# Performance work log

Hardware: AMD Instinct MI355X
Metric: run time of the kernel (lower is better)

## Reference

```python
import jax, jax.numpy as jnp
import numpy as np
import math

S, B, D = 2048, 8, 256
HEADS = 8
DPROJ = 128
DFF = 1024
DH = DPROJ // HEADS  # 16


def _layernorm(x, g, b, eps=1e-5):
    mu = jnp.mean(x, axis=-1, keepdims=True)
    var = jnp.mean((x - mu) ** 2, axis=-1, keepdims=True)
    return (x - mu) * jax.lax.rsqrt(var + eps) * g + b


def setup_inputs() -> dict:
    key = jax.random.key(0)
    ks = jax.random.split(key, 16)
    s = 0.02
    return {
        "src": jax.random.normal(ks[0], (S, B, D), dtype=jnp.float32),
        "Wq": jax.random.normal(ks[1], (D, DPROJ), dtype=jnp.float32) * s,
        "bq": jnp.zeros((DPROJ,), dtype=jnp.float32),
        "Wk": jax.random.normal(ks[2], (D, DPROJ), dtype=jnp.float32) * s,
        "bk": jnp.zeros((DPROJ,), dtype=jnp.float32),
        "Wv": jax.random.normal(ks[3], (D, DPROJ), dtype=jnp.float32) * s,
        "bv": jnp.zeros((DPROJ,), dtype=jnp.float32),
        "Wo": jax.random.normal(ks[4], (DPROJ, D), dtype=jnp.float32) * s,
        "ln1_g": jnp.ones((D,), dtype=jnp.float32),
        "ln1_b": jnp.zeros((D,), dtype=jnp.float32),
        "W1": jax.random.normal(ks[5], (D, DFF), dtype=jnp.float32) * s,
        "b1": jnp.zeros((DFF,), dtype=jnp.float32),
        "W2": jax.random.normal(ks[6], (DFF, D), dtype=jnp.float32) * s,
        "b2": jnp.zeros((D,), dtype=jnp.float32),
        "ln2_g": jnp.ones((D,), dtype=jnp.float32),
        "ln2_b": jnp.zeros((D,), dtype=jnp.float32),
    }


def reference(src, Wq, bq, Wk, bk, Wv, bv, Wo, ln1_g, ln1_b, W1, b1, W2, b2, ln2_g, ln2_b):
    # src: (S, B, D)
    q = src @ Wq + bq  # (S, B, DPROJ)
    k = src @ Wk + bk
    v = src @ Wv + bv

    # _reshape_to_batches: (S, B, h*dh) -> (S, B*h, dh), then sdpa moves batch first
    def split_heads(x):
        return jnp.transpose(x.reshape(S, B * HEADS, DH), (1, 0, 2))  # (B*h, S, dh)

    qh, kh, vh = split_heads(q), split_heads(k), split_heads(v)
    scores = jnp.einsum('bid,bjd->bij', qh, kh) / math.sqrt(DH)  # (B*h, S, S)
    attn = jax.nn.softmax(scores, axis=-1)
    ctx = jnp.einsum('bij,bjd->bid', attn, vh)  # (B*h, S, dh)

    # _reshape_from_batches: (B*h, S, dh) -> (S, B, DPROJ)
    ctx = jnp.transpose(ctx, (1, 0, 2)).reshape(S, B, DPROJ)
    y = ctx @ Wo  # (S, B, D), no bias

    x = _layernorm(src + y, ln1_g, ln1_b)
    ffn = jax.nn.relu(x @ W1 + b1) @ W2 + b2
    return _layernorm(x + ffn, ln2_g, ln2_b)
```

## Files before the change

### kernel.cpp

```cpp
#include <hip/hip_runtime.h>
#include <math.h>

#define SLEN 2048
#define BATCH 8
#define DMODEL 256
#define HEADS 8
#define DPROJ 128
#define DFF 1024
#define DH 16
#define MROWS (SLEN*BATCH)

typedef unsigned short u16;
typedef unsigned int u32;
typedef __attribute__((ext_vector_type(8))) short short8;
typedef __attribute__((ext_vector_type(4))) float f32x4;
typedef __attribute__((ext_vector_type(16))) float f32x16;
typedef __attribute__((ext_vector_type(4))) unsigned short u16x4;

__device__ __forceinline__ u16 f2bf(float x) {
    union { float f; u32 u; } v; v.f = x;
    u32 r = v.u + 0x7FFFu + ((v.u >> 16) & 1u);
    return (u16)(r >> 16);
}
__device__ __forceinline__ float bf2f(u16 h) {
    union { u32 u; float f; } v; v.u = ((u32)h) << 16;
    return v.f;
}
__device__ __forceinline__ float fexp2(float x) { return __builtin_amdgcn_exp2f(x); }
__device__ __forceinline__ u32 pack_bf(float lo, float hi) {
    union { float f; u32 u; } a, b; a.f = lo; b.f = hi;
    return __builtin_amdgcn_perm(b.u, a.u, 0x07060302u);
}
__device__ __forceinline__ void gld16(const u16* g, u16* l) {
    __builtin_amdgcn_global_load_lds(
        (const __attribute__((address_space(1))) void*)g,
        (__attribute__((address_space(3))) void*)l, 16, 0, 0);
}

__global__ void prep_kernel(const float* __restrict__ src, u16* __restrict__ srcb,
                            const float* __restrict__ Wq, const float* __restrict__ Wk,
                            const float* __restrict__ Wv, const float* __restrict__ Wo,
                            const float* __restrict__ W1, const float* __restrict__ W2,
                            u16* __restrict__ WqT, u16* __restrict__ WkT,
                            u16* __restrict__ WvT, u16* __restrict__ WoT,
                            u16* __restrict__ W1T, u16* __restrict__ W2T) {
    if (blockIdx.x < 4096) {
        int idx = (blockIdx.x * 256 + threadIdx.x) * 4;
        float4 v = *(const float4*)(src + idx);
        u16x4 o;
        o.x = f2bf(v.x); o.y = f2bf(v.y); o.z = f2bf(v.z); o.w = f2bf(v.w);
        *(u16x4*)(srcb + idx) = o;
        return;
    }
    int i = (blockIdx.x - 4096) * 256 + threadIdx.x;
    if (i < 32768) {
        int n = i >> 8, k = i & 255;
        WqT[i] = f2bf(Wq[k * 128 + n]);
    } else if (i < 65536) {
        int j = i - 32768; int n = j >> 8, k = j & 255;
        WkT[j] = f2bf(Wk[k * 128 + n]);
    } else if (i < 98304) {
        int j = i - 65536; int n = j >> 8, k = j & 255;
        WvT[j] = f2bf(Wv[k * 128 + n]);
    } else if (i < 131072) {
        int j = i - 98304; int n = j >> 7, k = j & 127;
        WoT[j] = f2bf(Wo[k * 256 + n]);
    } else if (i < 393216) {
        int j = i - 131072; int n = j >> 8, k = j & 255;
        W1T[j] = f2bf(W1[k * 1024 + n]);
    } else if (i < 655360) {
        int j = i - 393216; int n = j >> 10, k = j & 1023;
        W2T[j] = f2bf(W2[k * 256 + n]);
    }
}

template<int BN, bool RELU, bool HAS_BIAS, bool OUT_BF16>
__global__ void mfma_gemm(const u16* __restrict__ A, const u16* __restrict__ BT,
                          const float* __restrict__ bias, void* __restrict__ Cout,
                          int M, int N, int K) {
    constexpr int NJ = BN / 32;
    __shared__ __align__(16) u16 As[128 * 32];
    __shared__ __align__(16) u16 Bs[BN * 32];
    const int tid = threadIdx.x;
    const int row0 = blockIdx.x * 128;
    const int col0 = blockIdx.y * BN;
    const int w = tid >> 6, l = tid & 63;
    const int wr = (w & 1) * 64, wc = (w >> 1) * (BN / 2);
    const int lcol = l & 15, lrow = (l >> 4) * 4, g = l >> 4;
    const int sl = l >> 2;
    const int swc = ((l & 3) ^ (sl & 3)) * 8;
    const int fsw = (g ^ (lcol & 3)) * 8;

    const u16* Ag0 = A + (size_t)(row0 + 16 * w + sl) * K + swc;
    const u16* Ag1 = Ag0 + (size_t)64 * K;
    const u16* Bg0 = BT + (size_t)(col0 + 16 * w + sl) * K + swc;
    const u16* Bg1 = Bg0 + (size_t)64 * K;
    u16* lA0 = As + (16 * w) * 32;
    u16* lA1 = As + (16 * w + 64) * 32;
    u16* lB0 = Bs + (16 * w) * 32;
    u16* lB1 = Bs + (16 * w + 64) * 32;

    f32x4 acc[4][NJ] = {};
    for (int k0 = 0; k0 < K; k0 += 32) {
        gld16(Ag0 + k0, lA0);
        gld16(Ag1 + k0, lA1);
        gld16(Bg0 + k0, lB0);
        if (BN == 128) gld16(Bg1 + k0, lB1);
        __syncthreads();
        short8 af[4], bf[NJ];
        #pragma unroll
        for (int i = 0; i < 4; ++i)
            af[i] = *(const short8*)(As + (wr + i * 16 + lcol) * 32 + fsw);
        #pragma unroll
        for (int j = 0; j < NJ; ++j)
            bf[j] = *(const short8*)(Bs + (wc + j * 16 + lcol) * 32 + fsw);
        #pragma unroll
        for (int i = 0; i < 4; ++i)
            #pragma unroll
            for (int j = 0; j < NJ; ++j)
                acc[i][j] = __builtin_amdgcn_mfma_f32_16x16x32_bf16(
                    af[i], bf[j], acc[i][j], 0, 0, 0);
        __syncthreads();
    }
    float bv[NJ];
    #pragma unroll
    for (int j = 0; j < NJ; ++j)
        bv[j] = HAS_BIAS ? bias[col0 + wc + j * 16 + lcol] : 0.f;
    #pragma unroll
    for (int i = 0; i < 4; ++i) {
        #pragma unroll
        for (int r = 0; r < 4; ++r) {
            size_t grow = row0 + wr + i * 16 + lrow + r;
            #pragma unroll
            for (int j = 0; j < NJ; ++j) {
                int gcol = col0 + wc + j * 16 + lcol;
                float c = acc[i][j][r] + bv[j];
                if (RELU) c = fmaxf(c, 0.f);
                if (OUT_BF16) ((u16*)Cout)[grow * N + gcol] = f2bf(c);
                else          ((float*)Cout)[grow * N + gcol] = c;
            }
        }
    }
}

__global__ void qkv_mfma(const u16* __restrict__ A,
                         const u16* __restrict__ WqT, const u16* __restrict__ WkT,
                         const u16* __restrict__ WvT,
                         const float* __restrict__ bq, const float* __restrict__ bk,
                         const float* __restrict__ bv,
                         u16* __restrict__ qhp, u16* __restrict__ khp,
                         u16* __restrict__ vhb) {
    const int which = blockIdx.z;
    const u16* BT   = which == 0 ? WqT : (which == 1 ? WkT : WvT);
    const float* bs = which == 0 ? bq : (which == 1 ? bk : bv);
    u16* outp       = which == 0 ? qhp : (which == 1 ? khp : vhb);
    const float scale = which == 0 ? 0.25f * 1.44269504f : 1.0f;
    __shared__ __align__(16) u16 As[128 * 32];
    __shared__ __align__(16) u16 Bs[128 * 32];
    const int tid = threadIdx.x;
    const int row0 = blockIdx.x * 128;
    const int w = tid >> 6, l = tid & 63;
    const int wr = (w & 1) * 64, wc = (w >> 1) * 64;
    const int lcol = l & 15, lrow = (l >> 4) * 4, g = l >> 4;
    const int sl = l >> 2;
    const int swc = ((l & 3) ^ (sl & 3)) * 8;
    const int fsw = (g ^ (lcol & 3)) * 8;

    const u16* Ag0 = A + (size_t)(row0 + 16 * w + sl) * DMODEL + swc;
    const u16* Ag1 = Ag0 + (size_t)64 * DMODEL;
    const u16* Bg0 = BT + (size_t)(16 * w + sl) * DMODEL + swc;
    const u16* Bg1 = Bg0 + (size_t)64 * DMODEL;
    u16* lA0 = As + (16 * w) * 32;
    u16* lA1 = As + (16 * w + 64) * 32;
    u16* lB0 = Bs + (16 * w) * 32;
    u16* lB1 = Bs + (16 * w + 64) * 32;

    f32x4 acc[4][4] = {};
    for (int k0 = 0; k0 < DMODEL; k0 += 32) {
        gld16(Ag0 + k0, lA0);
        gld16(Ag1 + k0, lA1);
        gld16(Bg0 + k0, lB0);
        gld16(Bg1 + k0, lB1);
        __syncthreads();
        short8 af[4], bf[4];
        #pragma unroll
        for (int i = 0; i < 4; ++i)
            af[i] = *(const short8*)(As + (wr + i * 16 + lcol) * 32 + fsw);
        #pragma unroll
        for (int j = 0; j < 4; ++j)
            bf[j] = *(const short8*)(Bs + (wc + j * 16 + lcol) * 32 + fsw);
        #pragma unroll
        for (int i = 0; i < 4; ++i)
            #pragma unroll
            for (int j = 0; j < 4; ++j)
                acc[i][j] = __builtin_amdgcn_mfma_f32_16x16x32_bf16(
                    af[i], bf[j], acc[i][j], 0, 0, 0);
        __syncthreads();
    }
    #pragma unroll
    for (int i = 0; i < 4; ++i) {
        #pragma unroll
        for (int r = 0; r < 4; ++r) {
            int grow = row0 + wr + i * 16 + lrow + r;
            int b = grow & 7, s = grow >> 3;
            #pragma unroll
            for (int j = 0; j < 4; ++j) {
                int gcol = wc + j * 16 + lcol;
                int h = gcol >> 4, d = gcol & 15;
                float c = acc[i][j][r] + bs[gcol];
                outp[((size_t)(b * 8 + h) * SLEN + s) * 16 + d] = f2bf(c * scale);
            }
        }
    }
}

__global__ void transpose_v(const u16* __restrict__ vhb, u16* __restrict__ va) {
    __shared__ u16 T[128 * 24];
    const int bh = blockIdx.y;
    const int c0 = blockIdx.x * 128;
    const int t = threadIdx.x;
    {
        int key = t >> 1, half = t & 1;
        *(uint4*)(T + key * 24 + half * 8) =
            *(const uint4*)(vhb + ((size_t)bh * SLEN + c0 + key) * 16 + half * 8);
    }
    __syncthreads();
    int d = t >> 4, k8 = (t & 15) * 8;
    u16x4 o0, o1;
    o0.x = T[(k8 + 0) * 24 + d]; o0.y = T[(k8 + 1) * 24 + d];
    o0.z = T[(k8 + 2) * 24 + d]; o0.w = T[(k8 + 3) * 24 + d];
    o1.x = T[(k8 + 4) * 24 + d]; o1.y = T[(k8 + 5) * 24 + d];
    o1.z = T[(k8 + 6) * 24 + d]; o1.w = T[(k8 + 7) * 24 + d];
    u16* dst = va + ((size_t)bh * 32 + d) * SLEN + c0 + k8;
    *(u16x4*)dst = o0;
    *(u16x4*)(dst + 4) = o1;
    if (t < 16) {
        u16x4 ones = { (u16)0x3F80, (u16)0x3F80, (u16)0x3F80, (u16)0x3F80 };
        u16* od = va + ((size_t)bh * 32 + 16) * SLEN + c0 + t * 8;
        *(u16x4*)od = ones;
        *(u16x4*)(od + 4) = ones;
    }
}

__global__ __launch_bounds__(256, 4)
void attn_mfma(const u16* __restrict__ qg, const u16* __restrict__ kg,
               const u16* __restrict__ va, u16* __restrict__ ctx) {
    __shared__ __align__(16) u16 Ps[4 * 2 * 32 * 72];
    const int bh = blockIdx.y;
    const int q0 = blockIdx.x * 128;
    const int tid = threadIdx.x;
    const int w = tid >> 6, l = tid & 63;
    const int n = l & 31, h5 = l >> 5;
    u16* Pbase = Ps + w * (2 * 32 * 72);

    const short8 qf = *(const short8*)(
        qg + ((size_t)bh * SLEN + q0 + w * 32 + n) * 16 + h5 * 8);
    const u16* kb = kg + (size_t)bh * SLEN * 16;
    const u16* vb = va + ((size_t)bh * 32 + n) * SLEN + h5 * 8;

    f32x16 oacc = {};

    short8 kf0 = *(const short8*)(kb + (size_t)n * 16 + h5 * 8);
    short8 kf1 = *(const short8*)(kb + (size_t)(32 + n) * 16 + h5 * 8);

    for (int kt = 0; kt < 32; ++kt) {
        const int k0 = kt * 64;
        u16* Pw = Pbase + (kt & 1) * (32 * 72);
        short8 vf[4];
        #pragma unroll
        for (int st = 0; st < 4; ++st)
            vf[st] = *(const short8*)(vb + k0 + st * 16);
        f32x16 z = {};
        f32x16 s0 = __builtin_amdgcn_mfma_f32_32x32x16_bf16(kf0, qf, z, 0, 0, 0);
        f32x16 s1 = __builtin_amdgcn_mfma_f32_32x32x16_bf16(kf1, qf, z, 0, 0, 0);
        const int kn = (kt < 31) ? (k0 + 64) : 0;
        kf0 = *(const short8*)(kb + (size_t)(kn + n) * 16 + h5 * 8);
        kf1 = *(const short8*)(kb + (size_t)(kn + 32 + n) * 16 + h5 * 8);
        #pragma unroll
        for (int r4 = 0; r4 < 4; ++r4) {
            uint2 d0, d1;
            d0.x = pack_bf(fexp2(s0[r4 * 4 + 0]), fexp2(s0[r4 * 4 + 1]));
            d0.y = pack_bf(fexp2(s0[r4 * 4 + 2]), fexp2(s0[r4 * 4 + 3]));
            d1.x = pack_bf(fexp2(s1[r4 * 4 + 0]), fexp2(s1[r4 * 4 + 1]));
            d1.y = pack_bf(fexp2(s1[r4 * 4 + 2]), fexp2(s1[r4 * 4 + 3]));
            int kbase = 8 * r4 + 4 * h5;
            *(uint2*)(Pw + n * 72 + kbase) = d0;
            *(uint2*)(Pw + n * 72 + 32 + kbase) = d1;
        }
        #pragma unroll
        for (int st = 0; st < 4; ++st) {
            short8 ap = *(const short8*)(Pw + n * 72 + st * 16 + h5 * 8);
            oacc = __builtin_amdgcn_mfma_f32_32x32x16_bf16(ap, vf[st], oacc, 0, 0, 0);
        }
    }
    float* Ob = (float*)Pbase;
    #pragma unroll
    for (int r = 0; r < 16; ++r) {
        int q = (r & 3) + 8 * (r >> 2) + 4 * h5;
        if (n <= 16) Ob[q * 36 + n] = oacc[r];
    }
    __syncthreads();
    const int q = l >> 1, half = l & 1;
    f32x4 o0 = *(const f32x4*)(Ob + q * 36 + half * 8);
    f32x4 o1 = *(const f32x4*)(Ob + q * 36 + half * 8 + 4);
    float rcpL = 1.0f / Ob[q * 36 + 16];
    u16x4 pa, pb;
    pa.x = f2bf(o0[0] * rcpL); pa.y = f2bf(o0[1] * rcpL);
    pa.z = f2bf(o0[2] * rcpL); pa.w = f2bf(o0[3] * rcpL);
    pb.x = f2bf(o1[0] * rcpL); pb.y = f2bf(o1[1] * rcpL);
    pb.z = f2bf(o1[2] * rcpL); pb.w = f2bf(o1[3] * rcpL);
    const int b = bh >> 3, h = bh & 7;
    const int qrow = q0 + w * 32 + q;
    u16* dst = ctx + ((size_t)qrow * BATCH + b) * DPROJ + h * DH + half * 8;
    *(u16x4*)dst = pa;
    *(u16x4*)(dst + 4) = pb;
}

__global__ void ln1_kernel(const float* __restrict__ src, const u16* __restrict__ y,
                           const float* __restrict__ g, const float* __restrict__ bb,
                           u16* __restrict__ xb) {
    const int w = threadIdx.x >> 6, l = threadIdx.x & 63;
    const int row = blockIdx.x * 4 + w;
    const int c = l * 4;
    size_t base = (size_t)row * DMODEL;
    float4 s4 = *(const float4*)(src + base + c);
    u16x4 y4 = *(const u16x4*)(y + base + c);
    float v[4] = { s4.x + bf2f(y4.x), s4.y + bf2f(y4.y),
                   s4.z + bf2f(y4.z), s4.w + bf2f(y4.w) };
    float sum = v[0] + v[1] + v[2] + v[3];
    float ss  = v[0]*v[0] + v[1]*v[1] + v[2]*v[2] + v[3]*v[3];
    #pragma unroll
    for (int off = 1; off < 64; off <<= 1) {
        sum += __shfl_xor(sum, off);
        ss  += __shfl_xor(ss, off);
    }
    float mu = sum * (1.0f / 256.0f);
    float var = ss * (1.0f / 256.0f) - mu * mu;
    float rs = rsqrtf(var + 1e-5f);
    float4 g4 = *(const float4*)(g + c);
    float4 b4 = *(const float4*)(bb + c);
    u16x4 o;
    o.x = f2bf((v[0] - mu) * rs * g4.x + b4.x);
    o.y = f2bf((v[1] - mu) * rs * g4.y + b4.y);
    o.z = f2bf((v[2] - mu) * rs * g4.z + b4.z);
    o.w = f2bf((v[3] - mu) * rs * g4.w + b4.w);
    *(u16x4*)(xb + base + c) = o;
}

__global__ void ln2_kernel(const u16* __restrict__ x, const u16* __restrict__ f,
                           const float* __restrict__ g, const float* __restrict__ bb,
                           float* __restrict__ out) {
    const int w = threadIdx.x >> 6, l = threadIdx.x & 63;
    const int row = blockIdx.x * 4 + w;
    const int c = l * 4;
    size_t base = (size_t)row * DMODEL;
    u16x4 x4 = *(const u16x4*)(x + base + c);
    u16x4 f4 = *(const u16x4*)(f + base + c);
    float v[4] = { bf2f(x4.x) + bf2f(f4.x), bf2f(x4.y) + bf2f(f4.y),
                   bf2f(x4.z) + bf2f(f4.z), bf2f(x4.w) + bf2f(f4.w) };
    float sum = v[0] + v[1] + v[2] + v[3];
    float ss  = v[0]*v[0] + v[1]*v[1] + v[2]*v[2] + v[3]*v[3];
    #pragma unroll
    for (int off = 1; off < 64; off <<= 1) {
        sum += __shfl_xor(sum, off);
        ss  += __shfl_xor(ss, off);
    }
    float mu = sum * (1.0f / 256.0f);
    float var = ss * (1.0f / 256.0f) - mu * mu;
    float rs = rsqrtf(var + 1e-5f);
    float4 g4 = *(const float4*)(g + c);
    float4 b4 = *(const float4*)(bb + c);
    float4 o;
    o.x = (v[0] - mu) * rs * g4.x + b4.x;
    o.y = (v[1] - mu) * rs * g4.y + b4.y;
    o.z = (v[2] - mu) * rs * g4.z + b4.z;
    o.w = (v[3] - mu) * rs * g4.w + b4.w;
    *(float4*)(out + base + c) = o;
}

extern "C" void kernel_launch(void* const* d_in, const int* in_sizes, int n_in,
                              void* d_out, int out_size, void* d_ws, size_t ws_size,
                              hipStream_t stream) {
    const float* src = (const float*)d_in[0];
    const float* Wq  = (const float*)d_in[1];
    const float* bq  = (const float*)d_in[2];
    const float* Wk  = (const float*)d_in[3];
    const float* bk  = (const float*)d_in[4];
    const float* Wv  = (const float*)d_in[5];
    const float* bv  = (const float*)d_in[6];
    const float* Wo  = (const float*)d_in[7];
    const float* g1  = (const float*)d_in[8];
    const float* be1 = (const float*)d_in[9];
    const float* W1  = (const float*)d_in[10];
    const float* b1  = (const float*)d_in[11];
    const float* W2  = (const float*)d_in[12];
    const float* b2  = (const float*)d_in[13];
    const float* g2  = (const float*)d_in[14];
    const float* be2 = (const float*)d_in[15];
    char* ws = (char*)d_ws;
    float* out = (float*)d_out;

    u16* qhp  = (u16*)(ws + 0);
    u16* khp  = (u16*)(ws + 4194304);
    u16* vhb  = (u16*)(ws + 8388608);
    u16* vaug = (u16*)(ws + 12582912);
    u16* ctxb = (u16*)(ws + 20971520);
    u16* yb   = (u16*)(ws + 25165824);
    u16* hb   = (u16*)(ws + 0);
    u16* xb   = (u16*)(ws + 33554432);
    u16* fb   = (u16*)(ws + 41943040);
    u16* srcb = (u16*)(ws + 50331648);
    u16* WqT  = (u16*)(ws + 58720256);
    u16* WkT  = (u16*)(ws + 58785792);
    u16* WvT  = (u16*)(ws + 58851328);
    u16* WoT  = (u16*)(ws + 58916864);
    u16* W1T  = (u16*)(ws + 58982400);
    u16* W2T  = (u16*)(ws + 59506688);

    prep_kernel<<<6656, 256, 0, stream>>>(src, srcb, Wq, Wk, Wv, Wo, W1, W2,
                                          WqT, WkT, WvT, WoT, W1T, W2T);
    qkv_mfma<<<dim3(128, 1, 3), 256, 0, stream>>>(srcb, WqT, WkT, WvT,
                                                  bq, bk, bv, qhp, khp, vhb);
    transpose_v<<<dim3(16, 64), 256, 0, stream>>>(vhb, vaug);
    attn_mfma<<<dim3(16, 64), 256, 0, stream>>>(qhp, khp, vaug, ctxb);
    mfma_gemm<64, false, false, true><<<dim3(128, 4), 256, 0, stream>>>(
        ctxb, WoT, nullptr, yb, MROWS, DMODEL, DPROJ);
    ln1_kernel<<<MROWS / 4, 256, 0, stream>>>(src, yb, g1, be1, xb);
    mfma_gemm<128, true, true, true><<<dim3(128, 8), 256, 0, stream>>>(
        xb, W1T, b1, hb, MROWS, DFF, DMODEL);
    mfma_gemm<64, false, true, true><<<dim3(128, 4), 256, 0, stream>>>(
        hb, W2T, b2, fb, MROWS, DMODEL, DFF);
    ln2_kernel<<<MROWS / 4, 256, 0, stream>>>(xb, fb, g2, be2, out);
}
```

Baseline: 240.4 us.

## Split attention over key halves and combine fp32 partials in separate kernel

```diff
diff --git a/kernel.cpp b/kernel.cpp
--- a/kernel.cpp
+++ b/kernel.cpp
@@ -9,6 +9,7 @@
 #define DFF 1024
 #define DH 16
 #define MROWS (SLEN*BATCH)
+#define NROWS (SLEN*BATCH*8)
 
 typedef unsigned short u16;
 typedef unsigned int u32;
@@ -242,30 +243,30 @@
     }
 }
 
-__global__ __launch_bounds__(256, 4)
+__global__ __launch_bounds__(128, 8)
 void attn_mfma(const u16* __restrict__ qg, const u16* __restrict__ kg,
-               const u16* __restrict__ va, u16* __restrict__ ctx) {
-    __shared__ __align__(16) u16 Ps[4 * 2 * 32 * 72];
+               const u16* __restrict__ va, float* __restrict__ part) {
+    __shared__ __align__(16) u16 Ps[2 * 32 * 68];
     const int bh = blockIdx.y;
-    const int q0 = blockIdx.x * 128;
+    const int sl = blockIdx.z;
     const int tid = threadIdx.x;
     const int w = tid >> 6, l = tid & 63;
     const int n = l & 31, h5 = l >> 5;
-    u16* Pbase = Ps + w * (2 * 32 * 72);
-
+    u16* Pw = Ps + w * (32 * 68);
+
+    const int qbase = blockIdx.x * 64 + w * 32;
     const short8 qf = *(const short8*)(
-        qg + ((size_t)bh * SLEN + q0 + w * 32 + n) * 16 + h5 * 8);
+        qg + ((size_t)bh * SLEN + qbase + n) * 16 + h5 * 8);
     const u16* kb = kg + (size_t)bh * SLEN * 16;
     const u16* vb = va + ((size_t)bh * 32 + n) * SLEN + h5 * 8;
+    const int k00 = sl * (SLEN / 2);
 
     f32x16 oacc = {};
-
-    short8 kf0 = *(const short8*)(kb + (size_t)n * 16 + h5 * 8);
-    short8 kf1 = *(const short8*)(kb + (size_t)(32 + n) * 16 + h5 * 8);
-
-    for (int kt = 0; kt < 32; ++kt) {
-        const int k0 = kt * 64;
-        u16* Pw = Pbase + (kt & 1) * (32 * 72);
+    short8 kf0 = *(const short8*)(kb + (size_t)(k00 + n) * 16 + h5 * 8);
+    short8 kf1 = *(const short8*)(kb + (size_t)(k00 + 32 + n) * 16 + h5 * 8);
+
+    for (int kt = 0; kt < 16; ++kt) {
+        const int k0 = k00 + kt * 64;
         short8 vf[4];
         #pragma unroll
         for (int st = 0; st < 4; ++st)
@@ -273,47 +274,61 @@
         f32x16 z = {};
         f32x16 s0 = __builtin_amdgcn_mfma_f32_32x32x16_bf16(kf0, qf, z, 0, 0, 0);
         f32x16 s1 = __builtin_amdgcn_mfma_f32_32x32x16_bf16(kf1, qf, z, 0, 0, 0);
-        const int kn = (kt < 31) ? (k0 + 64) : 0;
+        const int kn = k00 + ((kt + 1) & 15) * 64;
         kf0 = *(const short8*)(kb + (size_t)(kn + n) * 16 + h5 * 8);
         kf1 = *(const short8*)(kb + (size_t)(kn + 32 + n) * 16 + h5 * 8);
         #pragma unroll
         for (int r4 = 0; r4 < 4; ++r4) {
-            uint2 d0, d1;
-            d0.x = pack_bf(fexp2(s0[r4 * 4 + 0]), fexp2(s0[r4 * 4 + 1]));
-            d0.y = pack_bf(fexp2(s0[r4 * 4 + 2]), fexp2(s0[r4 * 4 + 3]));
-            d1.x = pack_bf(fexp2(s1[r4 * 4 + 0]), fexp2(s1[r4 * 4 + 1]));
-            d1.y = pack_bf(fexp2(s1[r4 * 4 + 2]), fexp2(s1[r4 * 4 + 3]));
-            int kbase = 8 * r4 + 4 * h5;
-            *(uint2*)(Pw + n * 72 + kbase) = d0;
-            *(uint2*)(Pw + n * 72 + 32 + kbase) = d1;
+            uint2 d;
+            d.x = pack_bf(fexp2(s0[r4 * 4 + 0]), fexp2(s0[r4 * 4 + 1]));
+            d.y = pack_bf(fexp2(s0[r4 * 4 + 2]), fexp2(s0[r4 * 4 + 3]));
+            *(uint2*)(Pw + n * 68 + 8 * r4 + 4 * h5) = d;
+        }
+        #pragma unroll
+        for (int r4 = 0; r4 < 4; ++r4) {
+            uint2 d;
+            d.x = pack_bf(fexp2(s1[r4 * 4 + 0]), fexp2(s1[r4 * 4 + 1]));
+            d.y = pack_bf(fexp2(s1[r4 * 4 + 2]), fexp2(s1[r4 * 4 + 3]));
+            *(uint2*)(Pw + n * 68 + 32 + 8 * r4 + 4 * h5) = d;
         }
         #pragma unroll
         for (int st = 0; st < 4; ++st) {
-            short8 ap = *(const short8*)(Pw + n * 72 + st * 16 + h5 * 8);
-            oacc = __builtin_amdgcn_mfma_f32_32x32x16_bf16(ap, vf[st], oacc, 0, 0, 0);
-        }
-    }
-    float* Ob = (float*)Pbase;
-    #pragma unroll
-    for (int r = 0; r < 16; ++r) {
-        int q = (r & 3) + 8 * (r >> 2) + 4 * h5;
-        if (n <= 16) Ob[q * 36 + n] = oacc[r];
-    }
-    __syncthreads();
-    const int q = l >> 1, half = l & 1;
-    f32x4 o0 = *(const f32x4*)(Ob + q * 36 + half * 8);
-    f32x4 o1 = *(const f32x4*)(Ob + q * 36 + half * 8 + 4);
-    float rcpL = 1.0f / Ob[q * 36 + 16];
-    u16x4 pa, pb;
-    pa.x = f2bf(o0[0] * rcpL); pa.y = f2bf(o0[1] * rcpL);
-    pa.z = f2bf(o0[2] * rcpL); pa.w = f2bf(o0[3] * rcpL);
-    pb.x = f2bf(o1[0] * rcpL); pb.y = f2bf(o1[1] * rcpL);
-    pb.z = f2bf(o1[2] * rcpL); pb.w = f2bf(o1[3] * rcpL);
-    const int b = bh >> 3, h = bh & 7;
-    const int qrow = q0 + w * 32 + q;
-    u16* dst = ctx + ((size_t)qrow * BATCH + b) * DPROJ + h * DH + half * 8;
-    *(u16x4*)dst = pa;
-    *(u16x4*)(dst + 4) = pb;
+            const u16* rp = Pw + n * 68 + st * 16 + h5 * 8;
+            union { uint2 q2[2]; short8 v; } ap;
+            ap.q2[0] = *(const uint2*)rp;
+            ap.q2[1] = *(const uint2*)(rp + 4);
+            oacc = __builtin_amdgcn_mfma_f32_32x32x16_bf16(ap.v, vf[st], oacc, 0, 0, 0);
+        }
+    }
+    float* pr = part + ((size_t)sl * NROWS + (size_t)bh * SLEN + qbase) * 20;
+    if (n <= 16) {
+        #pragma unroll
+        for (int r = 0; r < 16; ++r) {
+            int qq = (r & 3) + 8 * (r >> 2) + 4 * h5;
+            pr[(size_t)qq * 20 + n] = oacc[r];
+        }
+    }
+}
+
+__global__ void attn_combine(const float* __restrict__ part, u16* __restrict__ ctx) {
+    int idx = blockIdx.x * 256 + threadIdx.x;
+    int row = idx >> 1, half = idx & 1;
+    const float* b0 = part + (size_t)row * 20;
+    const float* b1 = b0 + (size_t)NROWS * 20;
+    f32x4 a0 = *(const f32x4*)(b0 + half * 8);
+    f32x4 a1 = *(const f32x4*)(b0 + half * 8 + 4);
+    f32x4 c0 = *(const f32x4*)(b1 + half * 8);
+    f32x4 c1 = *(const f32x4*)(b1 + half * 8 + 4);
+    float rcp = 1.0f / (b0[16] + b1[16]);
+    u16x4 p0, p1;
+    p0.x = f2bf((a0[0] + c0[0]) * rcp); p0.y = f2bf((a0[1] + c0[1]) * rcp);
+    p0.z = f2bf((a0[2] + c0[2]) * rcp); p0.w = f2bf((a0[3] + c0[3]) * rcp);
+    p1.x = f2bf((a1[0] + c1[0]) * rcp); p1.y = f2bf((a1[1] + c1[1]) * rcp);
+    p1.z = f2bf((a1[2] + c1[2]) * rcp); p1.w = f2bf((a1[3] + c1[3]) * rcp);
+    int bh = row >> 11, q = row & 2047, b = bh >> 3, h = bh & 7;
+    u16* dst = ctx + ((size_t)q * BATCH + b) * DPROJ + h * DH + half * 8;
+    *(u16x4*)dst = p0;
+    *(u16x4*)(dst + 4) = p1;
 }
 
 __global__ void ln1_kernel(const float* __restrict__ src, const u16* __restrict__ y,
@@ -400,29 +415,31 @@
     char* ws = (char*)d_ws;
     float* out = (float*)d_out;
 
-    u16* qhp  = (u16*)(ws + 0);
-    u16* khp  = (u16*)(ws + 4194304);
-    u16* vhb  = (u16*)(ws + 8388608);
-    u16* vaug = (u16*)(ws + 12582912);
-    u16* ctxb = (u16*)(ws + 20971520);
-    u16* yb   = (u16*)(ws + 25165824);
-    u16* hb   = (u16*)(ws + 0);
-    u16* xb   = (u16*)(ws + 33554432);
-    u16* fb   = (u16*)(ws + 41943040);
-    u16* srcb = (u16*)(ws + 50331648);
-    u16* WqT  = (u16*)(ws + 58720256);
-    u16* WkT  = (u16*)(ws + 58785792);
-    u16* WvT  = (u16*)(ws + 58851328);
-    u16* WoT  = (u16*)(ws + 58916864);
-    u16* W1T  = (u16*)(ws + 58982400);
-    u16* W2T  = (u16*)(ws + 59506688);
+    u16*   qhp  = (u16*)  (ws + 0);
+    u16*   khp  = (u16*)  (ws + 4194304);
+    u16*   vhb  = (u16*)  (ws + 8388608);
+    u16*   vaug = (u16*)  (ws + 12582912);
+    float* part = (float*)(ws + 20971520);
+    u16*   ctxb = (u16*)  (ws + 41943040);
+    u16*   yb   = (u16*)  (ws + 46137344);
+    u16*   hb   = (u16*)  (ws + 0);
+    u16*   xb   = (u16*)  (ws + 54525952);
+    u16*   fb   = (u16*)  (ws + 62914560);
+    u16*   srcb = (u16*)  (ws + 71303168);
+    u16*   WqT  = (u16*)  (ws + 79691776);
+    u16*   WkT  = (u16*)  (ws + 79757312);
+    u16*   WvT  = (u16*)  (ws + 79822848);
+    u16*   WoT  = (u16*)  (ws + 79888384);
+    u16*   W1T  = (u16*)  (ws + 79953920);
+    u16*   W2T  = (u16*)  (ws + 80478208);
 
     prep_kernel<<<6656, 256, 0, stream>>>(src, srcb, Wq, Wk, Wv, Wo, W1, W2,
                                           WqT, WkT, WvT, WoT, W1T, W2T);
     qkv_mfma<<<dim3(128, 1, 3), 256, 0, stream>>>(srcb, WqT, WkT, WvT,
                                                   bq, bk, bv, qhp, khp, vhb);
     transpose_v<<<dim3(16, 64), 256, 0, stream>>>(vhb, vaug);
-    attn_mfma<<<dim3(16, 64), 256, 0, stream>>>(qhp, khp, vaug, ctxb);
+    attn_mfma<<<dim3(32, 64, 2), 128, 0, stream>>>(qhp, khp, vaug, part);
+    attn_combine<<<1024, 256, 0, stream>>>(part, ctxb);
     mfma_gemm<64, false, false, true><<<dim3(128, 4), 256, 0, stream>>>(
         ctxb, WoT, nullptr, yb, MROWS, DMODEL, DPROJ);
     ln1_kernel<<<MROWS / 4, 256, 0, stream>>>(src, yb, g1, be1, xb);
```

New measurement: 299.0 us. 1.24x slower.
